# Optimization experiments

Measured on AMD Instinct MI355X. Metric: run time of the kernel, lower is better.

Reference implementation:

```python
import jax, jax.numpy as jnp
import numpy as np

B, S, E = 2, 2048, 2048
H, G = 16, 4
HD = E // H          # 128
GD = HD * G          # 512
NGH = H // G         # 4 (tile factor for K/V heads)


def setup_inputs() -> dict:
    key = jax.random.key(0)
    ks = jax.random.split(key, 6)
    sc = 0.02
    return {
        "x": jax.random.normal(ks[0], (B, S, E), dtype=jnp.float32),
        "mask": jnp.ones((B, S, S), dtype=jnp.int32),
        "Wq": jax.random.normal(ks[1], (E, E), dtype=jnp.float32) * sc,
        "bq": jnp.zeros((E,), dtype=jnp.float32),
        "Wk": jax.random.normal(ks[2], (E, GD), dtype=jnp.float32) * sc,
        "bk": jnp.zeros((GD,), dtype=jnp.float32),
        "Wv": jax.random.normal(ks[3], (E, GD), dtype=jnp.float32) * sc,
        "bv": jnp.zeros((GD,), dtype=jnp.float32),
        "Wo": jax.random.normal(ks[4], (E, E), dtype=jnp.float32) * sc,
        "bo": jnp.zeros((E,), dtype=jnp.float32),
    }


def reference(x, mask, Wq, bq, Wk, bk, Wv, bv, Wo, bo):
    b, s, _ = x.shape
    # projections
    q = x @ Wq + bq                                   # [B,S,E]
    k = x @ Wk + bk                                   # [B,S,GD]
    v = x @ Wv + bv                                   # [B,S,GD]
    q = q.reshape(b, s, H, HD).transpose(0, 2, 1, 3)  # [B,H,S,hd]
    k = k.reshape(b, s, G, HD).transpose(0, 2, 1, 3)  # [B,G,S,hd]
    v = v.reshape(b, s, G, HD).transpose(0, 2, 1, 3)
    # torch .repeat(1, NGH, 1, 1): tile groups -> head h uses group h % G
    k = jnp.tile(k, (1, NGH, 1, 1))                   # [B,H,S,hd]
    v = jnp.tile(v, (1, NGH, 1, 1))
    scale = 1.0 / np.sqrt(HD).astype(np.float32)
    scores = jnp.einsum("bhqd,bhkd->bhqk", q, k) * scale
    m = mask[:, None, :, :]                           # [B,1,S,S]
    scores = jnp.where(m == 0, jnp.float32(-10000.0), scores)
    attn = jax.nn.softmax(scores, axis=-1)
    out = jnp.einsum("bhqk,bhkd->bhqd", attn, v)      # [B,H,S,hd]
    out = out.transpose(0, 2, 1, 3).reshape(b, s, E)  # [B,S,E]
    return out @ Wo + bo
```

## Files before the change

### kernel.cpp

```cpp
#include <hip/hip_runtime.h>

#define B_ 2
#define S_ 2048
#define E_ 2048
#define H_ 16
#define G_ 4
#define HD_ 128
#define GD_ 512
#define KVLD_ 1024
#define QKVN_ 3072
#define M_ (B_*S_)

using u16 = unsigned short;
using u32 = unsigned int;
typedef __attribute__((ext_vector_type(8))) short short8;
typedef __attribute__((ext_vector_type(4))) float f32x4;

#define QSCL 0.12751891114f
#define MASKED_L2 (-14427.0f)

__device__ __forceinline__ u16 f2bf(float f) {
  union { float f; unsigned u; } v; v.f = f;
  unsigned r = v.u + 0x7fff + ((v.u >> 16) & 1);
  return (u16)(r >> 16);
}

__device__ __forceinline__ void async16(const void* g, void* l) {
  __builtin_amdgcn_global_load_lds((const __attribute__((address_space(1))) unsigned int*)g,
                                   (__attribute__((address_space(3))) unsigned int*)l, 16, 0, 0);
}

__global__ __launch_bounds__(256) void cast_f32_bf16(const float* __restrict__ in,
                                                     u16* __restrict__ out, int n4) {
  int i = blockIdx.x * 256 + threadIdx.x;
  if (i >= n4) return;
  float4 v = ((const float4*)in)[i];
  union { u16 o[4]; uint2 u; } pk;
  pk.o[0] = f2bf(v.x); pk.o[1] = f2bf(v.y); pk.o[2] = f2bf(v.z); pk.o[3] = f2bf(v.w);
  *(uint2*)(out + (size_t)i * 4) = pk.u;
}

__global__ __launch_bounds__(256) void concat_bias3(const float* __restrict__ a,
                                                    const float* __restrict__ b,
                                                    const float* __restrict__ c,
                                                    float* __restrict__ o) {
  int t = blockIdx.x * 256 + threadIdx.x;
  if (t < 2048) o[t] = a[t];
  else if (t < 2560) o[t] = b[t - 2048];
  else if (t < 3072) o[t] = c[t - 2560];
}

__global__ __launch_bounds__(256) void transpose_cast(const float* __restrict__ W,
                                                      u16* __restrict__ Wt, int K, int N) {
  __shared__ u16 tile[64 * 72];
  int n0 = blockIdx.x * 64, k0 = blockIdx.y * 64;
  int t = threadIdx.x;
  int row = t >> 2;
  int seg = t & 3;
  const float* src = W + (size_t)(k0 + row) * N + n0 + seg * 16;
  #pragma unroll
  for (int i = 0; i < 4; ++i) {
    float4 v = *(const float4*)(src + i * 4);
    int nl = seg * 16 + i * 4;
    tile[(nl + 0) * 72 + row] = f2bf(v.x);
    tile[(nl + 1) * 72 + row] = f2bf(v.y);
    tile[(nl + 2) * 72 + row] = f2bf(v.z);
    tile[(nl + 3) * 72 + row] = f2bf(v.w);
  }
  __syncthreads();
  int nl = t >> 2, s2 = t & 3;
  u16* dst = Wt + (size_t)(n0 + nl) * K + k0 + s2 * 16;
  *(uint4*)dst       = *(const uint4*)&tile[nl * 72 + s2 * 16];
  *(uint4*)(dst + 8) = *(const uint4*)&tile[nl * 72 + s2 * 16 + 8];
}

__global__ __launch_bounds__(256) void transpose_v(const u16* __restrict__ KVb, u16* __restrict__ Vtg) {
  __shared__ u16 tile[64 * 72];
  int kv0 = blockIdx.x * 64;
  int gn0 = blockIdx.y * 64;
  int t = threadIdx.x;
  int row = t >> 2, seg = t & 3;
  int prow = (row & 15) * 4 + (row >> 4);
  const u16* src = KVb + (size_t)(kv0 + row) * KVLD_ + 512 + gn0 + seg * 16;
  union { uint4 v; u16 s[8]; } a, b;
  a.v = *(const uint4*)src; b.v = *(const uint4*)(src + 8);
  #pragma unroll
  for (int j = 0; j < 8; ++j) tile[(seg * 16 + j) * 72 + prow] = a.s[j];
  #pragma unroll
  for (int j = 0; j < 8; ++j) tile[(seg * 16 + 8 + j) * 72 + prow] = b.s[j];
  __syncthreads();
  int gl = t >> 2, ks2 = t & 3;
  int bb = kv0 >> 11;
  int s0 = kv0 & 2047;
  int gn = gn0 + gl;
  u16* dst = Vtg + (size_t)(bb * 512 + gn) * S_ + s0 + ks2 * 16;
  *(uint4*)dst       = *(const uint4*)&tile[gl * 72 + ks2 * 16];
  *(uint4*)(dst + 8) = *(const uint4*)&tile[gl * 72 + ks2 * 16 + 8];
}

__global__ __launch_bounds__(256) void mask_flags(const int* __restrict__ mask, int* __restrict__ flags) {
  int idx = blockIdx.x * 4 + (threadIdx.x >> 6);
  int lane = threadIdx.x & 63;
  int bb = idx >> 12, rg = (idx >> 5) & 127, kt = idx & 31;
  const int* base = mask + ((size_t)bb * S_ + rg * 16) * S_ + kt * 64;
  int row = lane >> 2, c0 = (lane & 3) * 16;
  int ok = 1;
  #pragma unroll
  for (int i = 0; i < 4; ++i) {
    int4 v = *(const int4*)&base[(size_t)row * S_ + c0 + i * 4];
    ok &= (v.x != 0) & (v.y != 0) & (v.z != 0) & (v.w != 0);
  }
  ok = __all(ok) ? 1 : 0;
  if (lane == 0) flags[idx] = ok;
}

__global__ __launch_bounds__(256) void gemm_qkv(const u16* __restrict__ A, const u16* __restrict__ Bt,
                                                const float* __restrict__ bias,
                                                u16* __restrict__ Qb, u16* __restrict__ KVb, int K) {
  __shared__ u16 As[2][128 * 32];
  __shared__ u16 Bs[2][128 * 32];
  int nbx = gridDim.x;
  int bid = blockIdx.y * nbx + blockIdx.x;
  int chunk = (nbx * gridDim.y) >> 3;
  int swz = (bid & 7) * chunk + (bid >> 3);
  int n0 = (swz % nbx) * 128, m0 = (swz / nbx) * 128;
  int t = threadIdx.x;
  int w = t >> 6, lane = t & 63, c = lane & 15, q = lane >> 4;
  int wm = w & 1, wn = w >> 1;
  int r0 = t >> 2;
  int kcs = ((t & 3) ^ ((t >> 3) & 3)) * 8;
  const u16* Ag0 = A  + (size_t)(m0 + r0) * K + kcs;
  const u16* Ag1 = A  + (size_t)(m0 + 64 + r0) * K + kcs;
  const u16* Bg0 = Bt + (size_t)(n0 + r0) * K + kcs;
  const u16* Bg1 = Bt + (size_t)(n0 + 64 + r0) * K + kcs;
  int roff = (q ^ ((c >> 1) & 3)) * 8;
  f32x4 acc[4][4] = {};
  async16(Ag0, &As[0][t * 8]);
  async16(Ag1, &As[0][2048 + t * 8]);
  async16(Bg0, &Bs[0][t * 8]);
  async16(Bg1, &Bs[0][2048 + t * 8]);
  for (int k0 = 0; k0 < K; k0 += 32) {
    int cur = (k0 >> 5) & 1;
    __syncthreads();
    if (k0 + 32 < K) {
      async16(Ag0 + k0 + 32, &As[cur ^ 1][t * 8]);
      async16(Ag1 + k0 + 32, &As[cur ^ 1][2048 + t * 8]);
      async16(Bg0 + k0 + 32, &Bs[cur ^ 1][t * 8]);
      async16(Bg1 + k0 + 32, &Bs[cur ^ 1][2048 + t * 8]);
    }
    short8 af[4], bf[4];
    #pragma unroll
    for (int i = 0; i < 4; ++i) {
      af[i] = *(const short8*)&As[cur][(wm * 64 + i * 16 + c) * 32 + roff];
      bf[i] = *(const short8*)&Bs[cur][(wn * 64 + i * 16 + c) * 32 + roff];
    }
    #pragma unroll
    for (int i = 0; i < 4; ++i)
      #pragma unroll
      for (int j = 0; j < 4; ++j)
        acc[i][j] = __builtin_amdgcn_mfma_f32_16x16x32_bf16(af[i], bf[j], acc[i][j], 0, 0, 0);
  }
  int isq = (n0 < 2048);
  #pragma unroll
  for (int i = 0; i < 4; ++i) {
    int mrow_base = m0 + wm * 64 + i * 16 + q * 4;
    #pragma unroll
    for (int j = 0; j < 4; ++j) {
      int coln = n0 + wn * 64 + j * 16 + c;
      float bv = bias[coln];
      #pragma unroll
      for (int r = 0; r < 4; ++r) {
        float v = acc[i][j][r] + bv;
        if (isq) Qb[(size_t)(mrow_base + r) * E_ + coln] = f2bf(v * QSCL);
        else     KVb[(size_t)(mrow_base + r) * KVLD_ + coln - 2048] = f2bf(v);
      }
    }
  }
}

__global__ __launch_bounds__(256) void gemm_k(const u16* __restrict__ A, const u16* __restrict__ Bt,
                                              const float* __restrict__ bias, float* __restrict__ Cout,
                                              int M, int N, int K) {
  __shared__ u16 As[2][128 * 32];
  __shared__ u16 Bs[2][128 * 32];
  int nbx = gridDim.x;
  int bid = blockIdx.y * nbx + blockIdx.x;
  int chunk = (nbx * gridDim.y) >> 3;
  int swz = (bid & 7) * chunk + (bid >> 3);
  int n0 = (swz % nbx) * 128, m0 = (swz / nbx) * 128;
  int t = threadIdx.x;
  int w = t >> 6, lane = t & 63, c = lane & 15, q = lane >> 4;
  int wm = w & 1, wn = w >> 1;
  int r0 = t >> 2;
  int kcs = ((t & 3) ^ ((t >> 3) & 3)) * 8;
  const u16* Ag0 = A  + (size_t)(m0 + r0) * K + kcs;
  const u16* Ag1 = A  + (size_t)(m0 + 64 + r0) * K + kcs;
  const u16* Bg0 = Bt + (size_t)(n0 + r0) * K + kcs;
  const u16* Bg1 = Bt + (size_t)(n0 + 64 + r0) * K + kcs;
  int roff = (q ^ ((c >> 1) & 3)) * 8;
  f32x4 acc[4][4] = {};
  async16(Ag0, &As[0][t * 8]);
  async16(Ag1, &As[0][2048 + t * 8]);
  async16(Bg0, &Bs[0][t * 8]);
  async16(Bg1, &Bs[0][2048 + t * 8]);
  for (int k0 = 0; k0 < K; k0 += 32) {
    int cur = (k0 >> 5) & 1;
    __syncthreads();
    if (k0 + 32 < K) {
      async16(Ag0 + k0 + 32, &As[cur ^ 1][t * 8]);
      async16(Ag1 + k0 + 32, &As[cur ^ 1][2048 + t * 8]);
      async16(Bg0 + k0 + 32, &Bs[cur ^ 1][t * 8]);
      async16(Bg1 + k0 + 32, &Bs[cur ^ 1][2048 + t * 8]);
    }
    short8 af[4], bf[4];
    #pragma unroll
    for (int i = 0; i < 4; ++i) {
      af[i] = *(const short8*)&As[cur][(wm * 64 + i * 16 + c) * 32 + roff];
      bf[i] = *(const short8*)&Bs[cur][(wn * 64 + i * 16 + c) * 32 + roff];
    }
    #pragma unroll
    for (int i = 0; i < 4; ++i)
      #pragma unroll
      for (int j = 0; j < 4; ++j)
        acc[i][j] = __builtin_amdgcn_mfma_f32_16x16x32_bf16(af[i], bf[j], acc[i][j], 0, 0, 0);
  }
  #pragma unroll
  for (int i = 0; i < 4; ++i) {
    int mrow_base = m0 + wm * 64 + i * 16 + q * 4;
    #pragma unroll
    for (int j = 0; j < 4; ++j) {
      int coln = n0 + wn * 64 + j * 16 + c;
      float bv = bias[coln];
      #pragma unroll
      for (int r = 0; r < 4; ++r)
        Cout[(size_t)(mrow_base + r) * N + coln] = acc[i][j][r] + bv;
    }
  }
}

__global__ __launch_bounds__(512) void attn_k(const u16* __restrict__ Q, const u16* __restrict__ KVb,
                                              const u16* __restrict__ Vtg, const int* __restrict__ mask,
                                              const int* __restrict__ mflags, u16* __restrict__ O) {
  __shared__ u16 Ks[2][64 * 128];
  __shared__ u16 Vs[2][128 * 64];
  __shared__ u16 Ps[8 * 16 * 64];
  int bid = blockIdx.x;
  int mt = bid & 15, h = (bid >> 4) & 15, bb = bid >> 8;
  int g = h & 3;
  int t = threadIdx.x, w = t >> 6, lane = t & 63, c = lane & 15, q = lane >> 4;
  int m0 = mt * 128;

  const u16* Qbase  = Q   + (size_t)(bb * S_ + m0) * E_ + h * HD_;
  const u16* Kbase  = KVb + (size_t)bb * S_ * KVLD_ + g * HD_;
  const u16* Vtbase = Vtg + (size_t)(bb * G_ + g) * HD_ * S_;

  int krow0 = t >> 4;
  int kkc   = ((t & 15) ^ (krow0 & 15)) * 8;
  const u16* Kst = Kbase + (size_t)krow0 * KVLD_ + kkc;
  int vn0 = t >> 3;
  int vkc = ((t & 7) ^ (vn0 & 7)) * 8;
  const u16* Vst = Vtbase + (size_t)vn0 * S_ + vkc;

  int pwa[4], pra[2];
  #pragma unroll
  for (int r = 0; r < 4; ++r) {
    int row = q * 4 + r;
    pwa[r] = w * 1024 + row * 64 + (((c >> 1) ^ (row & 7)) * 8) + (c & 1) * 4;
  }
  #pragma unroll
  for (int ks = 0; ks < 2; ++ks)
    pra[ks] = w * 1024 + c * 64 + (((ks * 4 + q) ^ (c & 7)) * 8);

  short8 aq[4];
  #pragma unroll
  for (int k0 = 0; k0 < 4; ++k0)
    aq[k0] = *(const short8*)&Qbase[(size_t)(w * 16 + c) * E_ + k0 * 32 + q * 8];

  const short8 ones = {(short)0x3F80, (short)0x3F80, (short)0x3F80, (short)0x3F80,
                       (short)0x3F80, (short)0x3F80, (short)0x3F80, (short)0x3F80};

  f32x4 Oa[8] = {};
  f32x4 lacc = {};

  #pragma unroll
  for (int p = 0; p < 2; ++p)
    async16(Kst + (size_t)(p * 32) * KVLD_, &Ks[0][p * 4096 + t * 8]);
  #pragma unroll
  for (int p = 0; p < 2; ++p)
    async16(Vst + (size_t)(p * 64) * S_, &Vs[0][p * 4096 + t * 8]);

  for (int kv0 = 0; kv0 < S_; kv0 += 64) {
    int cur = (kv0 >> 6) & 1;
    __syncthreads();
    if (kv0 + 64 < S_) {
      #pragma unroll
      for (int p = 0; p < 2; ++p)
        async16(Kst + (size_t)(kv0 + 64 + p * 32) * KVLD_, &Ks[cur ^ 1][p * 4096 + t * 8]);
      #pragma unroll
      for (int p = 0; p < 2; ++p)
        async16(Vst + (size_t)(p * 64) * S_ + kv0 + 64, &Vs[cur ^ 1][p * 4096 + t * 8]);
    }
    const u16* K_ = Ks[cur];
    const u16* V_ = Vs[cur];

    f32x4 sc[4] = {};
    #pragma unroll
    for (int k0 = 0; k0 < 4; ++k0) {
      short8 bk[4];
      #pragma unroll
      for (int ns = 0; ns < 4; ++ns)
        bk[ns] = *(const short8*)&K_[(ns * 16 + c) * 128 + (((k0 * 4 + q) ^ c) * 8)];
      #pragma unroll
      for (int ns = 0; ns < 4; ++ns)
        sc[ns] = __builtin_amdgcn_mfma_f32_16x16x32_bf16(aq[k0], bk[ns], sc[ns], 0, 0, 0);
    }
    {
      int flag = mflags[bb * 4096 + (mt * 8 + w) * 32 + (kv0 >> 6)];
      if (!flag) {
        #pragma unroll
        for (int r = 0; r < 4; ++r) {
          int qrow = m0 + w * 16 + q * 4 + r;
          const int* mrow = mask + ((size_t)bb * S_ + qrow) * S_ + kv0;
          #pragma unroll
          for (int ns = 0; ns < 4; ++ns)
            if (mrow[ns * 16 + c] == 0) sc[ns][r] = MASKED_L2;
        }
      }
    }
    #pragma unroll
    for (int r = 0; r < 4; ++r) {
      u32 u[4];
      #pragma unroll
      for (int ns = 0; ns < 4; ++ns) {
        float p = __builtin_amdgcn_exp2f(sc[ns][r]);
        u[ns] = __float_as_uint(p) + 0x8000u;
      }
      uint2 pk;
      pk.x = __builtin_amdgcn_perm(u[1], u[0], 0x07060302);
      pk.y = __builtin_amdgcn_perm(u[3], u[2], 0x07060302);
      *(uint2*)&Ps[pwa[r]] = pk;
    }
    __asm__ volatile("" ::: "memory");
    #pragma unroll
    for (int ks = 0; ks < 2; ++ks) {
      short8 ap = *(const short8*)&Ps[pra[ks]];
      lacc = __builtin_amdgcn_mfma_f32_16x16x32_bf16(ap, ones, lacc, 0, 0, 0);
      #pragma unroll
      for (int d = 0; d < 8; ++d) {
        short8 bv = *(const short8*)&V_[(d * 16 + c) * 64 + (((ks * 4 + q) ^ (c & 7)) * 8)];
        Oa[d] = __builtin_amdgcn_mfma_f32_16x16x32_bf16(ap, bv, Oa[d], 0, 0, 0);
      }
    }
  }
  {
    float inv[4];
    #pragma unroll
    for (int r = 0; r < 4; ++r) inv[r] = 1.0f / lacc[r];
    #pragma unroll
    for (int d = 0; d < 8; ++d)
      #pragma unroll
      for (int r = 0; r < 4; ++r) {
        size_t off = (size_t)(bb * S_ + m0 + w * 16 + q * 4 + r) * E_ + h * HD_ + d * 16 + c;
        O[off] = f2bf(Oa[d][r] * inv[r]);
      }
  }
}

extern "C" void kernel_launch(void* const* d_in, const int* in_sizes, int n_in,
                              void* d_out, int out_size, void* d_ws, size_t ws_size,
                              hipStream_t stream) {
  const float* x    = (const float*)d_in[0];
  const int*   mask = (const int*)d_in[1];
  const float* Wq   = (const float*)d_in[2];
  const float* bq   = (const float*)d_in[3];
  const float* Wk   = (const float*)d_in[4];
  const float* bk   = (const float*)d_in[5];
  const float* Wv   = (const float*)d_in[6];
  const float* bv   = (const float*)d_in[7];
  const float* Wo   = (const float*)d_in[8];
  const float* bo   = (const float*)d_in[9];
  float* out = (float*)d_out;

  char* ws = (char*)d_ws;
  u16* xb    = (u16*)ws; ws += (size_t)M_ * E_ * 2;
  u16* Wqkvt = (u16*)ws; ws += (size_t)QKVN_ * E_ * 2;
  u16* Wot   = (u16*)ws; ws += (size_t)E_ * E_ * 2;
  u16* Qb    = (u16*)ws; ws += (size_t)M_ * E_ * 2;
  u16* KVb   = (u16*)ws; ws += (size_t)M_ * KVLD_ * 2;
  u16* Ob    = (u16*)ws; ws += (size_t)M_ * E_ * 2;
  u16* Vtg   = (u16*)ws; ws += (size_t)B_ * G_ * HD_ * S_ * 2;
  int* mfl   = (int*)ws; ws += (size_t)B_ * 128 * 32 * 4;
  float* bqkv = (float*)ws; ws += QKVN_ * 4;

  cast_f32_bf16<<<(M_ * E_ / 4 + 255) / 256, 256, 0, stream>>>(x, xb, M_ * E_ / 4);
  transpose_cast<<<dim3(E_ / 64,  E_ / 64), 256, 0, stream>>>(Wq, Wqkvt, E_, E_);
  transpose_cast<<<dim3(GD_ / 64, E_ / 64), 256, 0, stream>>>(Wk, Wqkvt + (size_t)2048 * E_, E_, GD_);
  transpose_cast<<<dim3(GD_ / 64, E_ / 64), 256, 0, stream>>>(Wv, Wqkvt + (size_t)2560 * E_, E_, GD_);
  transpose_cast<<<dim3(E_ / 64,  E_ / 64), 256, 0, stream>>>(Wo, Wot, E_, E_);
  concat_bias3<<<QKVN_ / 256, 256, 0, stream>>>(bq, bk, bv, bqkv);
  mask_flags<<<B_ * 128 * 32 / 4, 256, 0, stream>>>(mask, mfl);

  gemm_qkv<<<dim3(QKVN_ / 128, M_ / 128), 256, 0, stream>>>(xb, Wqkvt, bqkv, Qb, KVb, E_);
  transpose_v<<<dim3(M_ / 64, GD_ / 64), 256, 0, stream>>>(KVb, Vtg);

  attn_k<<<B_ * H_ * (S_ / 128), 512, 0, stream>>>(Qb, KVb, Vtg, mask, mfl, Ob);

  gemm_k<<<dim3(E_ / 128, M_ / 128), 256, 0, stream>>>(Ob, Wot, bo, out, M_, E_, E_);
}
```

Baseline: 351.2 us.

## Switch attention kernel to 32x32x16 MFMA with 4 waves of 32 rows

```diff
diff --git a/kernel.cpp b/kernel.cpp
--- a/kernel.cpp
+++ b/kernel.cpp
@@ -13,8 +13,10 @@
 
 using u16 = unsigned short;
 using u32 = unsigned int;
+typedef __attribute__((ext_vector_type(4))) short s16x4;
 typedef __attribute__((ext_vector_type(8))) short short8;
 typedef __attribute__((ext_vector_type(4))) float f32x4;
+typedef __attribute__((ext_vector_type(16))) float f32x16;
 
 #define QSCL 0.12751891114f
 #define MASKED_L2 (-14427.0f)
@@ -80,7 +82,7 @@
   int gn0 = blockIdx.y * 64;
   int t = threadIdx.x;
   int row = t >> 2, seg = t & 3;
-  int prow = (row & 15) * 4 + (row >> 4);
+  int prow = (row & 31) * 2 + (row >> 5);
   const u16* src = KVb + (size_t)(kv0 + row) * KVLD_ + 512 + gn0 + seg * 16;
   union { uint4 v; u16 s[8]; } a, b;
   a.v = *(const uint4*)src; b.v = *(const uint4*)(src + 8);
@@ -238,16 +240,17 @@
   }
 }
 
-__global__ __launch_bounds__(512) void attn_k(const u16* __restrict__ Q, const u16* __restrict__ KVb,
+__global__ __launch_bounds__(256) void attn_k(const u16* __restrict__ Q, const u16* __restrict__ KVb,
                                               const u16* __restrict__ Vtg, const int* __restrict__ mask,
                                               const int* __restrict__ mflags, u16* __restrict__ O) {
   __shared__ u16 Ks[2][64 * 128];
   __shared__ u16 Vs[2][128 * 64];
-  __shared__ u16 Ps[8 * 16 * 64];
+  __shared__ u16 Ps[4 * 32 * 64];
   int bid = blockIdx.x;
   int mt = bid & 15, h = (bid >> 4) & 15, bb = bid >> 8;
   int g = h & 3;
-  int t = threadIdx.x, w = t >> 6, lane = t & 63, c = lane & 15, q = lane >> 4;
+  int t = threadIdx.x, w = t >> 6, lane = t & 63;
+  int l31 = lane & 31, hi = lane >> 5;
   int m0 = mt * 128;
 
   const u16* Qbase  = Q   + (size_t)(bb * S_ + m0) * E_ + h * HD_;
@@ -255,114 +258,105 @@
   const u16* Vtbase = Vtg + (size_t)(bb * G_ + g) * HD_ * S_;
 
   int krow0 = t >> 4;
-  int kkc   = ((t & 15) ^ (krow0 & 15)) * 8;
+  int kkc   = ((t & 15) ^ (t >> 4)) * 8;
   const u16* Kst = Kbase + (size_t)krow0 * KVLD_ + kkc;
   int vn0 = t >> 3;
-  int vkc = ((t & 7) ^ (vn0 & 7)) * 8;
+  int vkc = ((t & 7) ^ ((t >> 3) & 7)) * 8;
   const u16* Vst = Vtbase + (size_t)vn0 * S_ + vkc;
 
-  int pwa[4], pra[2];
-  #pragma unroll
-  for (int r = 0; r < 4; ++r) {
-    int row = q * 4 + r;
-    pwa[r] = w * 1024 + row * 64 + (((c >> 1) ^ (row & 7)) * 8) + (c & 1) * 4;
-  }
-  #pragma unroll
-  for (int ks = 0; ks < 2; ++ks)
-    pra[ks] = w * 1024 + c * 64 + (((ks * 4 + q) ^ (c & 7)) * 8);
-
-  short8 aq[4];
-  #pragma unroll
-  for (int k0 = 0; k0 < 4; ++k0)
-    aq[k0] = *(const short8*)&Qbase[(size_t)(w * 16 + c) * E_ + k0 * 32 + q * 8];
+  int pwa[16], pra[8];
+  #pragma unroll
+  for (int reg = 0; reg < 16; ++reg) {
+    int row = (reg & 3) + 8 * (reg >> 2) + 4 * hi;
+    pwa[reg] = w * 2048 + row * 64 + (((l31 >> 1) ^ (row & 15)) << 2) + ((l31 & 1) << 1);
+  }
+  #pragma unroll
+  for (int k = 0; k < 8; ++k)
+    pra[k] = w * 2048 + l31 * 64 + ((((k >> 1) * 4 + hi * 2 + (k & 1)) ^ (l31 & 15)) << 2);
+
+  short8 aq[8];
+  #pragma unroll
+  for (int k0 = 0; k0 < 8; ++k0)
+    aq[k0] = *(const short8*)&Qbase[(size_t)(w * 32 + l31) * E_ + k0 * 16 + hi * 8];
 
   const short8 ones = {(short)0x3F80, (short)0x3F80, (short)0x3F80, (short)0x3F80,
                        (short)0x3F80, (short)0x3F80, (short)0x3F80, (short)0x3F80};
 
-  f32x4 Oa[8] = {};
-  f32x4 lacc = {};
-
-  #pragma unroll
-  for (int p = 0; p < 2; ++p)
-    async16(Kst + (size_t)(p * 32) * KVLD_, &Ks[0][p * 4096 + t * 8]);
-  #pragma unroll
-  for (int p = 0; p < 2; ++p)
-    async16(Vst + (size_t)(p * 64) * S_, &Vs[0][p * 4096 + t * 8]);
+  f32x16 Oa[4] = {};
+  f32x16 lacc = {};
+
+  #pragma unroll
+  for (int p = 0; p < 4; ++p)
+    async16(Kst + (size_t)(p * 16) * KVLD_, &Ks[0][p * 2048 + t * 8]);
+  #pragma unroll
+  for (int p = 0; p < 4; ++p)
+    async16(Vst + (size_t)(p * 32) * S_, &Vs[0][p * 2048 + t * 8]);
 
   for (int kv0 = 0; kv0 < S_; kv0 += 64) {
     int cur = (kv0 >> 6) & 1;
     __syncthreads();
     if (kv0 + 64 < S_) {
       #pragma unroll
-      for (int p = 0; p < 2; ++p)
-        async16(Kst + (size_t)(kv0 + 64 + p * 32) * KVLD_, &Ks[cur ^ 1][p * 4096 + t * 8]);
-      #pragma unroll
-      for (int p = 0; p < 2; ++p)
-        async16(Vst + (size_t)(p * 64) * S_ + kv0 + 64, &Vs[cur ^ 1][p * 4096 + t * 8]);
+      for (int p = 0; p < 4; ++p)
+        async16(Kst + (size_t)(kv0 + 64 + p * 16) * KVLD_, &Ks[cur ^ 1][p * 2048 + t * 8]);
+      #pragma unroll
+      for (int p = 0; p < 4; ++p)
+        async16(Vst + (size_t)(p * 32) * S_ + kv0 + 64, &Vs[cur ^ 1][p * 2048 + t * 8]);
     }
     const u16* K_ = Ks[cur];
     const u16* V_ = Vs[cur];
 
-    f32x4 sc[4] = {};
-    #pragma unroll
-    for (int k0 = 0; k0 < 4; ++k0) {
-      short8 bk[4];
-      #pragma unroll
-      for (int ns = 0; ns < 4; ++ns)
-        bk[ns] = *(const short8*)&K_[(ns * 16 + c) * 128 + (((k0 * 4 + q) ^ c) * 8)];
-      #pragma unroll
-      for (int ns = 0; ns < 4; ++ns)
-        sc[ns] = __builtin_amdgcn_mfma_f32_16x16x32_bf16(aq[k0], bk[ns], sc[ns], 0, 0, 0);
+    f32x16 sc[2] = {};
+    #pragma unroll
+    for (int k0 = 0; k0 < 8; ++k0) {
+      int koff = (((k0 * 2 + hi) ^ (l31 & 15)) << 3);
+      short8 bk0 = *(const short8*)&K_[l31 * 128 + koff];
+      short8 bk1 = *(const short8*)&K_[(32 + l31) * 128 + koff];
+      sc[0] = __builtin_amdgcn_mfma_f32_32x32x16_bf16(aq[k0], bk0, sc[0], 0, 0, 0);
+      sc[1] = __builtin_amdgcn_mfma_f32_32x32x16_bf16(aq[k0], bk1, sc[1], 0, 0, 0);
     }
     {
-      int flag = mflags[bb * 4096 + (mt * 8 + w) * 32 + (kv0 >> 6)];
+      int fb = bb * 4096 + (mt * 8 + w * 2) * 32 + (kv0 >> 6);
+      int flag = mflags[fb] & mflags[fb + 32];
       if (!flag) {
         #pragma unroll
-        for (int r = 0; r < 4; ++r) {
-          int qrow = m0 + w * 16 + q * 4 + r;
+        for (int reg = 0; reg < 16; ++reg) {
+          int row = (reg & 3) + 8 * (reg >> 2) + 4 * hi;
+          int qrow = m0 + w * 32 + row;
           const int* mrow = mask + ((size_t)bb * S_ + qrow) * S_ + kv0;
-          #pragma unroll
-          for (int ns = 0; ns < 4; ++ns)
-            if (mrow[ns * 16 + c] == 0) sc[ns][r] = MASKED_L2;
+          if (mrow[l31] == 0)      sc[0][reg] = MASKED_L2;
+          if (mrow[32 + l31] == 0) sc[1][reg] = MASKED_L2;
         }
       }
     }
     #pragma unroll
-    for (int r = 0; r < 4; ++r) {
-      u32 u[4];
-      #pragma unroll
-      for (int ns = 0; ns < 4; ++ns) {
-        float p = __builtin_amdgcn_exp2f(sc[ns][r]);
-        u[ns] = __float_as_uint(p) + 0x8000u;
+    for (int reg = 0; reg < 16; ++reg) {
+      u32 u0 = __float_as_uint(__builtin_amdgcn_exp2f(sc[0][reg])) + 0x8000u;
+      u32 u1 = __float_as_uint(__builtin_amdgcn_exp2f(sc[1][reg])) + 0x8000u;
+      *(u32*)&Ps[pwa[reg]] = __builtin_amdgcn_perm(u1, u0, 0x07060302);
+    }
+    __asm__ volatile("" ::: "memory");
+    #pragma unroll
+    for (int ks = 0; ks < 4; ++ks) {
+      s16x4 plo = *(const s16x4*)&Ps[pra[ks * 2]];
+      s16x4 phi = *(const s16x4*)&Ps[pra[ks * 2 + 1]];
+      short8 ap = {plo[0], plo[1], plo[2], plo[3], phi[0], phi[1], phi[2], phi[3]};
+      lacc = __builtin_amdgcn_mfma_f32_32x32x16_bf16(ap, ones, lacc, 0, 0, 0);
+      #pragma unroll
+      for (int db = 0; db < 4; ++db) {
+        short8 bv = *(const short8*)&V_[(db * 32 + l31) * 64 + (((ks * 2 + hi) ^ (l31 & 7)) << 3)];
+        Oa[db] = __builtin_amdgcn_mfma_f32_32x32x16_bf16(ap, bv, Oa[db], 0, 0, 0);
       }
-      uint2 pk;
-      pk.x = __builtin_amdgcn_perm(u[1], u[0], 0x07060302);
-      pk.y = __builtin_amdgcn_perm(u[3], u[2], 0x07060302);
-      *(uint2*)&Ps[pwa[r]] = pk;
-    }
-    __asm__ volatile("" ::: "memory");
-    #pragma unroll
-    for (int ks = 0; ks < 2; ++ks) {
-      short8 ap = *(const short8*)&Ps[pra[ks]];
-      lacc = __builtin_amdgcn_mfma_f32_16x16x32_bf16(ap, ones, lacc, 0, 0, 0);
-      #pragma unroll
-      for (int d = 0; d < 8; ++d) {
-        short8 bv = *(const short8*)&V_[(d * 16 + c) * 64 + (((ks * 4 + q) ^ (c & 7)) * 8)];
-        Oa[d] = __builtin_amdgcn_mfma_f32_16x16x32_bf16(ap, bv, Oa[d], 0, 0, 0);
-      }
-    }
-  }
-  {
-    float inv[4];
-    #pragma unroll
-    for (int r = 0; r < 4; ++r) inv[r] = 1.0f / lacc[r];
-    #pragma unroll
-    for (int d = 0; d < 8; ++d)
-      #pragma unroll
-      for (int r = 0; r < 4; ++r) {
-        size_t off = (size_t)(bb * S_ + m0 + w * 16 + q * 4 + r) * E_ + h * HD_ + d * 16 + c;
-        O[off] = f2bf(Oa[d][r] * inv[r]);
-      }
+    }
+  }
+  #pragma unroll
+  for (int reg = 0; reg < 16; ++reg) {
+    float iv = 1.0f / lacc[reg];
+    int row = (reg & 3) + 8 * (reg >> 2) + 4 * hi;
+    size_t rbase = (size_t)(bb * S_ + m0 + w * 32 + row) * E_ + h * HD_ + l31;
+    #pragma unroll
+    for (int db = 0; db < 4; ++db)
+      O[rbase + db * 32] = f2bf(Oa[db][reg] * iv);
   }
 }
 
@@ -403,7 +397,7 @@
   gemm_qkv<<<dim3(QKVN_ / 128, M_ / 128), 256, 0, stream>>>(xb, Wqkvt, bqkv, Qb, KVb, E_);
   transpose_v<<<dim3(M_ / 64, GD_ / 64), 256, 0, stream>>>(KVb, Vtg);
 
-  attn_k<<<B_ * H_ * (S_ / 128), 512, 0, stream>>>(Qb, KVb, Vtg, mask, mfl, Ob);
+  attn_k<<<B_ * H_ * (S_ / 128), 256, 0, stream>>>(Qb, KVb, Vtg, mask, mfl, Ob);
 
   gemm_k<<<dim3(E_ / 128, M_ / 128), 256, 0, stream>>>(Ob, Wot, bo, out, M_, E_, E_);
 }
```

Measured after the change: 362.3 us. 3.2% more time.
